# Performance work log

Measured on AMD Instinct MI355X. Metric: run time of the kernel, lower is better.

Reference implementation:

```python
import jax, jax.numpy as jnp
import numpy as np

B, S, IN, D, H, K, NLVL = 8, 1536, 32, 128, 4, 7, 2
DFF = 4 * D
DK = D // H
EPS = 1e-6


def setup_inputs() -> dict:
    key = jax.random.key(0)
    ks = jax.random.split(key, 24)
    rn = lambda k, sh, s=0.05: jax.random.normal(k, sh, jnp.float32) * s
    z = lambda sh: jnp.zeros(sh, jnp.float32)
    o = lambda sh: jnp.ones(sh, jnp.float32)
    return {
        'x': jax.random.normal(ks[0], (B, S, IN), jnp.float32),
        'enc_W': rn(ks[1], (IN, D)), 'enc_b': z((D,)),
        'ln_rnn_a': o((NLVL, D)), 'ln_rnn_b': z((NLVL, D)),
        'gru_Wih': rn(ks[2], (NLVL, 3 * D, D)), 'gru_Whh': rn(ks[3], (NLVL, 3 * D, D)),
        'gru_bih': z((NLVL, 3 * D)), 'gru_bhh': z((NLVL, 3 * D)),
        'ln_attn_a': o((NLVL, D)), 'ln_attn_b': z((NLVL, D)),
        'Wq': rn(ks[4], (NLVL, D, D)), 'bq': z((NLVL, D)),
        'Wk': rn(ks[5], (NLVL, D, D)), 'bk': z((NLVL, D)),
        'Wv': rn(ks[6], (NLVL, D, D)), 'bv': z((NLVL, D)),
        'Wo': rn(ks[7], (NLVL, D, D)), 'bo': z((NLVL, D)),
        'ln_ff_a': o((NLVL, D)), 'ln_ff_b': z((NLVL, D)),
        'ff_W1': rn(ks[8], (NLVL, D, DFF)), 'ff_b1': z((NLVL, DFF)),
        'ff_W2': rn(ks[9], (NLVL, DFF, D)), 'ff_b2': z((NLVL, D)),
        'out_W': rn(ks[10], (D, 1)), 'out_b': z((1,)),
    }


def layernorm(x, a, b):
    # faithful to torch code: unbiased std (ddof=1), divide by (std + eps)
    m = x.mean(-1, keepdims=True)
    s = jnp.std(x, axis=-1, ddof=1, keepdims=True)
    return a * (x - m) / (s + EPS) + b


def local_rnn(x, Wih, Whh, bih, bhh):
    # x: [B,S,D]. Window each position into its ksize-length causal window,
    # run a GRU over the window (scan over K steps, batched over B*S), keep last h.
    xp = jnp.pad(x, ((0, 0), (K - 1, 0), (0, 0)))            # zero left-pad
    win = jnp.stack([xp[:, i:i + S] for i in range(K)], 0)   # [K,B,S,D]

    def step(h, xt):
        gi = xt @ Wih.T + bih                                 # [B,S,3D]
        gh = h @ Whh.T + bhh
        ir, iz, inn = jnp.split(gi, 3, -1)
        hr, hz, hn = jnp.split(gh, 3, -1)
        r = jax.nn.sigmoid(ir + hr)
        zz = jax.nn.sigmoid(iz + hz)
        nn_ = jnp.tanh(inn + r * hn)
        return (1.0 - zz) * nn_ + zz * h, None

    h, _ = jax.lax.scan(step, jnp.zeros_like(x), win)
    return h


def mhpool(x, Wq, bq, Wk, bk, Wv, bv, Wo, bo):
    def heads(w, bb):
        return jnp.swapaxes((x @ w + bb).reshape(B, S, H, DK), 1, 2)  # [B,H,S,DK]
    q, k, v = heads(Wq, bq), heads(Wk, bk), heads(Wv, bv)
    scores = jnp.einsum('bhqd,bhkd->bhqk', q, k) / np.float32(np.sqrt(DK))
    mask = jnp.tril(jnp.ones((S, S), bool))
    scores = jnp.where(mask, scores, jnp.float32(-1e9))
    p = jax.nn.softmax(scores, axis=-1)
    o = jnp.einsum('bhqk,bhkd->bhqd', p, v)
    o = jnp.swapaxes(o, 1, 2).reshape(B, S, D)
    return o @ Wo + bo


def reference(x, enc_W, enc_b, ln_rnn_a, ln_rnn_b, gru_Wih, gru_Whh, gru_bih,
              gru_bhh, ln_attn_a, ln_attn_b, Wq, bq, Wk, bk, Wv, bv, Wo, bo,
              ln_ff_a, ln_ff_b, ff_W1, ff_b1, ff_W2, ff_b2, out_W, out_b):
    h = x @ enc_W + enc_b
    for i in range(NLVL):
        # LocalRNNLayer (pre-norm residual); LocalRNN.output Linear is unused in orig forward
        h = h + local_rnn(layernorm(h, ln_rnn_a[i], ln_rnn_b[i]),
                          gru_Wih[i], gru_Whh[i], gru_bih[i], gru_bhh[i])
        # MHPooling sublayer
        h = h + mhpool(layernorm(h, ln_attn_a[i], ln_attn_b[i]),
                       Wq[i], bq[i], Wk[i], bk[i], Wv[i], bv[i], Wo[i], bo[i])
        # PositionwiseFeedForward sublayer
        hn = layernorm(h, ln_ff_a[i], ln_ff_b[i])
        h = h + (jax.nn.relu(hn @ ff_W1[i] + ff_b1[i]) @ ff_W2[i] + ff_b2[i])
    return jax.nn.sigmoid(h @ out_W + out_b)
```

## Files before the change

kernel.cpp:

```cpp
#include <hip/hip_runtime.h>
#include <math.h>

#define DEV_INLINE __device__ __forceinline__

constexpr int B = 8, S = 1536, IN = 32, D = 128, NH = 4, KWIN = 7, NLVL = 2;
constexpr int DFF = 512, DKH = 32;
constexpr int M = B * S;
constexpr int MD = M * D;
constexpr float EPS = 1e-6f;

typedef unsigned short u16;
typedef __bf16 bf16x8 __attribute__((ext_vector_type(8)));
typedef float f32x4 __attribute__((ext_vector_type(4)));
typedef unsigned short u16x4 __attribute__((ext_vector_type(4)));

#define MFMA16(a, b, c) __builtin_amdgcn_mfma_f32_16x16x32_bf16(a, b, c, 0, 0, 0)

DEV_INLINE float sigmoidf_(float x) { return 1.f / (1.f + __expf(-x)); }

DEV_INLINE u16 f2bf(float f) {
    unsigned u = __builtin_bit_cast(unsigned, f);
    unsigned rnd = 0x7FFFu + ((u >> 16) & 1u);
    return (u16)((u + rnd) >> 16);
}
DEV_INLINE float b2f(u16 v) { return __builtin_bit_cast(float, (unsigned)v << 16); }

template <int KDIM>
DEV_INLINE void mfma_tile32(const u16* a0p, const u16* a1p, const u16* b0p, const u16* b1p,
                            f32x4& acc00, f32x4& acc01, f32x4& acc10, f32x4& acc11) {
    #pragma unroll
    for (int k0 = 0; k0 < KDIM; k0 += 32) {
        bf16x8 a0 = *(const bf16x8*)(a0p + k0);
        bf16x8 a1 = *(const bf16x8*)(a1p + k0);
        bf16x8 b0 = *(const bf16x8*)(b0p + k0);
        bf16x8 b1 = *(const bf16x8*)(b1p + k0);
        acc00 = MFMA16(a0, b0, acc00);
        acc01 = MFMA16(a0, b1, acc01);
        acc10 = MFMA16(a1, b0, acc10);
        acc11 = MFMA16(a1, b1, acc11);
    }
}

__global__ void k_prep(const float* __restrict__ Wih, const float* __restrict__ Whh,
                       const float* __restrict__ Wq, const float* __restrict__ Wk,
                       const float* __restrict__ Wv, const float* __restrict__ Wo,
                       const float* __restrict__ W1, const float* __restrict__ W2,
                       u16* __restrict__ Wih16, u16* __restrict__ Whh16,
                       u16* __restrict__ Wqkv, u16* __restrict__ WoT,
                       u16* __restrict__ W1T, u16* __restrict__ W2T) {
    constexpr int SZ_GRU = NLVL * 384 * 128;
    constexpr int SZ_DD  = NLVL * 128 * 128;
    constexpr int SZ_FF  = NLVL * 128 * 512;
    int i = blockIdx.x * 256 + threadIdx.x;
    if (i < SZ_GRU) { Wih16[i] = f2bf(Wih[i]); return; }
    i -= SZ_GRU;
    if (i < SZ_GRU) { Whh16[i] = f2bf(Whh[i]); return; }
    i -= SZ_GRU;
    if (i < 3 * SZ_DD) {
        int seg = i / SZ_DD, j = i - seg * SZ_DD;
        int lvl = j >> 14, rem = j & 16383, k = rem >> 7, n = rem & 127;
        const float* src = seg == 0 ? Wq : (seg == 1 ? Wk : Wv);
        Wqkv[(size_t)lvl * 384 * 128 + (size_t)(seg * 128 + n) * 128 + k] = f2bf(src[j]);
        return;
    }
    i -= 3 * SZ_DD;
    if (i < SZ_DD) {
        int lvl = i >> 14, rem = i & 16383, k = rem >> 7, n = rem & 127;
        WoT[(size_t)lvl * 16384 + n * 128 + k] = f2bf(Wo[i]); return;
    }
    i -= SZ_DD;
    if (i < SZ_FF) {
        int lvl = i >> 16, rem = i & 65535, k = rem >> 9, n = rem & 511;
        W1T[(size_t)lvl * 65536 + n * 128 + k] = f2bf(W1[i]); return;
    }
    i -= SZ_FF;
    if (i < SZ_FF) {
        int lvl = i >> 16, rem = i & 65535, k = rem >> 7, n = rem & 127;
        W2T[(size_t)lvl * 65536 + n * 512 + k] = f2bf(W2[i]); return;
    }
}

__global__ __launch_bounds__(256) void k_encoder(
    const float* __restrict__ x, const float* __restrict__ W, const float* __restrict__ b,
    const float* __restrict__ ga, const float* __restrict__ gb,
    float* __restrict__ h, u16* __restrict__ xnout) {
    __shared__ float xs[32][33];
    __shared__ float Ws[32][128];
    const int tid = threadIdx.x;
    const int row0 = blockIdx.x * 32;
    for (int i = tid; i < 32 * 32; i += 256) xs[i >> 5][i & 31] = x[(size_t)row0 * IN + i];
    for (int i = tid; i < 32 * 128; i += 256) Ws[i >> 7][i & 127] = W[i];
    __syncthreads();
    const int r = tid >> 3, cg = (tid & 7) * 16;
    float acc[16];
    #pragma unroll
    for (int j = 0; j < 16; ++j) acc[j] = b[cg + j];
    for (int k = 0; k < IN; ++k) {
        const float xv = xs[r][k];
        #pragma unroll
        for (int j = 0; j < 16; ++j) acc[j] = fmaf(xv, Ws[k][cg + j], acc[j]);
    }
    float s = 0.f;
    #pragma unroll
    for (int j = 0; j < 16; ++j) s += acc[j];
    s += __shfl_xor(s, 1); s += __shfl_xor(s, 2); s += __shfl_xor(s, 4);
    const float mean = s * (1.f / D);
    float q = 0.f;
    #pragma unroll
    for (int j = 0; j < 16; ++j) { float d = acc[j] - mean; q += d * d; }
    q += __shfl_xor(q, 1); q += __shfl_xor(q, 2); q += __shfl_xor(q, 4);
    const float inv = 1.f / (sqrtf(q * (1.f / (D - 1))) + EPS);
    float* hp = h + (size_t)(row0 + r) * D + cg;
    u16* xp = xnout + (size_t)(row0 + r) * D + cg;
    #pragma unroll
    for (int jj = 0; jj < 4; ++jj) {
        float4 hv = make_float4(acc[4 * jj], acc[4 * jj + 1], acc[4 * jj + 2], acc[4 * jj + 3]);
        *(float4*)(hp + 4 * jj) = hv;
        u16x4 o;
        #pragma unroll
        for (int c = 0; c < 4; ++c)
            o[c] = f2bf(ga[cg + 4 * jj + c] * (acc[4 * jj + c] - mean) * inv + gb[cg + 4 * jj + c]);
        *(u16x4*)(xp + 4 * jj) = o;
    }
}

__global__ __launch_bounds__(256) void k_gemm_qkv(
    const u16* __restrict__ A, const u16* __restrict__ Bqkv,
    const float* __restrict__ bq, const float* __restrict__ bk, const float* __restrict__ bv,
    u16* __restrict__ q16, u16* __restrict__ k16, u16* __restrict__ vt16) {
    constexpr float QS = 0.17677669529663687f * 1.4426950408889634f;
    const int wave = threadIdx.x >> 6, lane = threadIdx.x & 63;
    const int col16 = lane & 15, quad = lane >> 4;
    const int row0 = (blockIdx.x * 4 + wave) * 32;
    const int seg = blockIdx.y >> 2;
    const int c0 = (blockIdx.y & 3) * 32;
    const u16* a0p = A + (size_t)(row0 + col16) * 128 + quad * 8;
    const u16* b0p = Bqkv + (size_t)(seg * 128 + c0 + col16) * 128 + quad * 8;
    f32x4 acc00 = {0.f, 0.f, 0.f, 0.f}, acc01 = acc00, acc10 = acc00, acc11 = acc00;
    mfma_tile32<128>(a0p, a0p + 16 * 128, b0p, b0p + 16 * 128, acc00, acc01, acc10, acc11);
    const float* bias = seg == 0 ? bq : (seg == 1 ? bk : bv);
    const float bv0 = bias[c0 + col16];
    const float bv1 = bias[c0 + 16 + col16];
    if (seg < 2) {
        const float sc = seg == 0 ? QS : 1.f;
        u16* o16 = seg == 0 ? q16 : k16;
        #pragma unroll
        for (int r = 0; r < 4; ++r) {
            const size_t r0 = (size_t)(row0 + quad * 4 + r) * 128;
            const size_t r1 = r0 + 16 * 128;
            o16[r0 + c0 + col16]      = f2bf((acc00[r] + bv0) * sc);
            o16[r0 + c0 + 16 + col16] = f2bf((acc01[r] + bv1) * sc);
            o16[r1 + c0 + col16]      = f2bf((acc10[r] + bv0) * sc);
            o16[r1 + c0 + 16 + col16] = f2bf((acc11[r] + bv1) * sc);
        }
    } else {
        const int bb = row0 / S;
        const int ssv = row0 - bb * S;
        const int ca = c0 + col16, cb = c0 + 16 + col16;
        u16* pa = vt16 + ((size_t)((bb * NH + (ca >> 5)) * 32 + (ca & 31))) * S + ssv;
        u16* pb = vt16 + ((size_t)((bb * NH + (cb >> 5)) * 32 + (cb & 31))) * S + ssv;
        #pragma unroll
        for (int r = 0; r < 4; ++r) {
            const int lr = quad * 4 + r;
            pa[lr]      = f2bf(acc00[r] + bv0);
            pb[lr]      = f2bf(acc01[r] + bv1);
            pa[lr + 16] = f2bf(acc10[r] + bv0);
            pb[lr + 16] = f2bf(acc11[r] + bv1);
        }
    }
}

__global__ __launch_bounds__(512, 2) void k_gru_fused(
    const u16* __restrict__ xn,
    const u16* __restrict__ Wih16,
    const u16* __restrict__ Whh16,
    const float* __restrict__ bih, const float* __restrict__ bhh,
    float* __restrict__ hout,
    const float* __restrict__ ga, const float* __restrict__ gb,
    u16* __restrict__ xnaout) {
    constexpr int RB = 48;
    __shared__ __align__(16) u16 xnS[64 * 136];
    __shared__ __align__(16) u16 Gs[64 * 392];
    __shared__ __align__(16) u16 hs16[RB * 136];
    const int tid = threadIdx.x;
    const int wave = tid >> 6, lane = tid & 63;
    const int col16 = lane & 15, quad = lane >> 4;
    const int row0 = blockIdx.x * RB;
    const int ss0 = row0 % S;
    const int cc = wave * 16 + col16;

    for (int i = tid; i < 64 * 16; i += 512) {
        const int r = i >> 4, c8 = (i & 15) * 8;
        bf16x8 val = {};
        if (ss0 - 16 + r >= 0)
            val = *(const bf16x8*)(xn + (size_t)(row0 - 16 + r) * 128 + c8);
        *(bf16x8*)&xnS[r * 136 + c8] = val;
    }
    bf16x8 Breg[3][4];
    #pragma unroll
    for (int g = 0; g < 3; ++g)
        #pragma unroll
        for (int kc = 0; kc < 4; ++kc)
            Breg[g][kc] = *(const bf16x8*)(Whh16 + (size_t)(g * 128 + cc) * 128 + kc * 32 + quad * 8);
    float bi[3], bh[3];
    #pragma unroll
    for (int g = 0; g < 3; ++g) { bi[g] = bih[g * 128 + cc]; bh[g] = bhh[g * 128 + cc]; }
    __syncthreads();

    #pragma unroll
    for (int tt = wave; tt < 24; tt += 8) {
        const int rt = tt / 12, ct = tt - rt * 12;
        const u16* bp = Wih16 + (size_t)(ct * 32 + col16) * 128 + quad * 8;
        f32x4 a00 = {0.f, 0.f, 0.f, 0.f}, a01 = a00, a10 = a00, a11 = a00;
        #pragma unroll
        for (int k0 = 0; k0 < 128; k0 += 32) {
            bf16x8 af0 = *(const bf16x8*)&xnS[(rt * 32 + col16) * 136 + k0 + quad * 8];
            bf16x8 af1 = *(const bf16x8*)&xnS[(rt * 32 + 16 + col16) * 136 + k0 + quad * 8];
            bf16x8 b0 = *(const bf16x8*)(bp + k0);
            bf16x8 b1 = *(const bf16x8*)(bp + 16 * 128 + k0);
            a00 = MFMA16(af0, b0, a00);
            a01 = MFMA16(af0, b1, a01);
            a10 = MFMA16(af1, b0, a10);
            a11 = MFMA16(af1, b1, a11);
        }
        #pragma unroll
        for (int r = 0; r < 4; ++r) {
            const int gr0 = rt * 32 + quad * 4 + r, gr1 = gr0 + 16;
            Gs[gr0 * 392 + ct * 32 + col16]      = f2bf(a00[r]);
            Gs[gr0 * 392 + ct * 32 + 16 + col16] = f2bf(a01[r]);
            Gs[gr1 * 392 + ct * 32 + col16]      = f2bf(a10[r]);
            Gs[gr1 * 392 + ct * 32 + 16 + col16] = f2bf(a11[r]);
        }
    }
    float hp[12] = {};
    __syncthreads();

    for (int t = 0; t < KWIN; ++t) {
        const int shift = KWIN - 1 - t;
        f32x4 acc[3][3];
        #pragma unroll
        for (int rh = 0; rh < 3; ++rh)
            #pragma unroll
            for (int g = 0; g < 3; ++g) acc[rh][g] = {0.f, 0.f, 0.f, 0.f};
        if (t > 0) {
            bf16x8 af[3][4];
            #pragma unroll
            for (int rh = 0; rh < 3; ++rh)
                #pragma unroll
                for (int kc = 0; kc < 4; ++kc)
                    af[rh][kc] = *(const bf16x8*)&hs16[(rh * 16 + col16) * 136 + kc * 32 + quad * 8];
            __syncthreads();
            #pragma unroll
            for (int kc = 0; kc < 4; ++kc)
                #pragma unroll
                for (int g = 0; g < 3; ++g)
                    #pragma unroll
                    for (int rh = 0; rh < 3; ++rh)
                        acc[rh][g] = MFMA16(af[rh][kc], Breg[g][kc], acc[rh][g]);
        }
        const bool last = (t == KWIN - 1);
        #pragma unroll
        for (int rh = 0; rh < 3; ++rh) {
            #pragma unroll
            for (int r = 0; r < 4; ++r) {
                const int idx = rh * 4 + r;
                const int lrow = rh * 16 + quad * 4 + r;
                const int gr = lrow - shift + 16;
                const float xr  = b2f(Gs[gr * 392 + cc]);
                const float xz  = b2f(Gs[gr * 392 + 128 + cc]);
                const float xn_ = b2f(Gs[gr * 392 + 256 + cc]);
                const float rr = sigmoidf_(xr + bi[0] + acc[rh][0][r] + bh[0]);
                const float zz = sigmoidf_(xz + bi[1] + acc[rh][1][r] + bh[1]);
                const float e2 = __expf(2.f * (xn_ + bi[2] + rr * (acc[rh][2][r] + bh[2])));
                const float nn = 1.f - 2.f / (e2 + 1.f);
                const float hnew = (1.f - zz) * nn + zz * hp[idx];
                hp[idx] = hnew;
                if (!last) hs16[lrow * 136 + cc] = f2bf(hnew);
            }
        }
        __syncthreads();
    }
    float* hf = (float*)Gs;
    #pragma unroll
    for (int rh = 0; rh < 3; ++rh)
        #pragma unroll
        for (int r = 0; r < 4; ++r) {
            const int lrow = rh * 16 + quad * 4 + r;
            const float hv = hp[rh * 4 + r] + hout[(size_t)(row0 + lrow) * D + cc];
            hout[(size_t)(row0 + lrow) * D + cc] = hv;
            hf[lrow * 132 + cc] = hv;
        }
    __syncthreads();
    const int r = tid >> 3;
    if (r < RB) {
        const int cg = (tid & 7) * 16;
        float vals[16];
        #pragma unroll
        for (int jj = 0; jj < 4; ++jj) {
            float4 v = *(const float4*)&hf[r * 132 + cg + 4 * jj];
            vals[4 * jj] = v.x; vals[4 * jj + 1] = v.y; vals[4 * jj + 2] = v.z; vals[4 * jj + 3] = v.w;
        }
        float s = 0.f;
        #pragma unroll
        for (int j = 0; j < 16; ++j) s += vals[j];
        s += __shfl_xor(s, 1); s += __shfl_xor(s, 2); s += __shfl_xor(s, 4);
        const float mean = s * (1.f / D);
        float q = 0.f;
        #pragma unroll
        for (int j = 0; j < 16; ++j) { float d = vals[j] - mean; q += d * d; }
        q += __shfl_xor(q, 1); q += __shfl_xor(q, 2); q += __shfl_xor(q, 4);
        const float inv = 1.f / (sqrtf(q * (1.f / (D - 1))) + EPS);
        u16* xp = xnaout + (size_t)(row0 + r) * D + cg;
        #pragma unroll
        for (int jj = 0; jj < 4; ++jj) {
            u16x4 o;
            #pragma unroll
            for (int c = 0; c < 4; ++c)
                o[c] = f2bf(ga[cg + 4 * jj + c] * (vals[4 * jj + c] - mean) * inv + gb[cg + 4 * jj + c]);
            *(u16x4*)(xp + 4 * jj) = o;
        }
    }
}

__global__ __launch_bounds__(256) void k_attn_mfma(
    const u16* Qb, const u16* __restrict__ Kb,
    const u16* __restrict__ Vt, u16* O16) {
    const int wave = threadIdx.x >> 6, lane = threadIdx.x & 63;
    const int p = blockIdx.x;
    const int bh = blockIdx.y;
    const int b = bh >> 2, hh = bh & 3;
    const int col = lane & 15, quad = lane >> 4;

    __shared__ __align__(16) u16 Pb[4][32][40];
    __shared__ float Om[4][32][33];
    __shared__ float Lm[4][32];
    u16 (* __restrict__ P)[40] = Pb[wave];

    const u16* Kbase = Kb + (size_t)b * S * 128 + hh * 32;
    const u16* Vbase = Vt + (size_t)bh * 32 * S;

    #pragma unroll
    for (int half = 0; half < 2; ++half) {
        const int qt = half == 0 ? p : 47 - p;
        const int q0 = qt * 32;
        const int nkt = qt + 1;
        const u16* qp = Qb + (size_t)(b * S + q0 + col) * 128 + hh * 32 + quad * 8;
        const bf16x8 qf0 = *(const bf16x8*)qp;
        const bf16x8 qf1 = *(const bf16x8*)(qp + 16 * 128);
        f32x4 o00 = {0.f, 0.f, 0.f, 0.f}, o01 = o00, o10 = o00, o11 = o00;
        float lsum[8] = {};
        int kt = wave;
        bf16x8 kf0 = {}, kf1 = {}, vf0 = {}, vf1 = {};
        if (kt < nkt) {
            const u16* kp = Kbase + (size_t)(kt * 32 + col) * 128 + quad * 8;
            kf0 = *(const bf16x8*)kp;
            kf1 = *(const bf16x8*)(kp + 16 * 128);
            const u16* vp = Vbase + (size_t)col * S + kt * 32 + quad * 8;
            vf0 = *(const bf16x8*)vp;
            vf1 = *(const bf16x8*)(vp + 16 * S);
        }
        while (kt < nkt) {
            const int ktn = kt + 4;
            bf16x8 nk0 = kf0, nk1 = kf1, nv0 = vf0, nv1 = vf1;
            if (ktn < nkt) {
                const u16* kp = Kbase + (size_t)(ktn * 32 + col) * 128 + quad * 8;
                nk0 = *(const bf16x8*)kp;
                nk1 = *(const bf16x8*)(kp + 16 * 128);
                const u16* vp = Vbase + (size_t)col * S + ktn * 32 + quad * 8;
                nv0 = *(const bf16x8*)vp;
                nv1 = *(const bf16x8*)(vp + 16 * S);
            }
            f32x4 z = {0.f, 0.f, 0.f, 0.f};
            f32x4 s00 = MFMA16(qf0, kf0, z);
            f32x4 s01 = MFMA16(qf0, kf1, z);
            f32x4 s10 = MFMA16(qf1, kf0, z);
            f32x4 s11 = MFMA16(qf1, kf1, z);
            const bool diag = (kt == qt);
            const int k0g = kt * 32;
            #pragma unroll
            for (int r = 0; r < 4; ++r) {
                const int lr = quad * 4 + r;
                float p00 = __builtin_amdgcn_exp2f(s00[r]);
                float p01 = __builtin_amdgcn_exp2f(s01[r]);
                float p10 = __builtin_amdgcn_exp2f(s10[r]);
                float p11 = __builtin_amdgcn_exp2f(s11[r]);
                if (diag) {
                    const int qg0 = q0 + lr, qg1 = q0 + 16 + lr;
                    if (k0g + col > qg0)      p00 = 0.f;
                    if (k0g + 16 + col > qg0) p01 = 0.f;
                    if (k0g + col > qg1)      p10 = 0.f;
                    if (k0g + 16 + col > qg1) p11 = 0.f;
                }
                lsum[r]     += p00 + p01;
                lsum[4 + r] += p10 + p11;
                P[lr][col]           = f2bf(p00);
                P[lr][16 + col]      = f2bf(p01);
                P[16 + lr][col]      = f2bf(p10);
                P[16 + lr][16 + col] = f2bf(p11);
            }
            const bf16x8 pa0 = *(const bf16x8*)&P[col][quad * 8];
            const bf16x8 pa1 = *(const bf16x8*)&P[16 + col][quad * 8];
            o00 = MFMA16(pa0, vf0, o00);
            o01 = MFMA16(pa0, vf1, o01);
            o10 = MFMA16(pa1, vf0, o10);
            o11 = MFMA16(pa1, vf1, o11);
            kf0 = nk0; kf1 = nk1; vf0 = nv0; vf1 = nv1;
            kt = ktn;
        }
        #pragma unroll
        for (int i = 0; i < 8; ++i) {
            float v = lsum[i];
            v += __shfl_xor(v, 1); v += __shfl_xor(v, 2);
            v += __shfl_xor(v, 4); v += __shfl_xor(v, 8);
            lsum[i] = v;
        }
        #pragma unroll
        for (int r = 0; r < 4; ++r) {
            const int lr = quad * 4 + r;
            Om[wave][lr][col]           = o00[r];
            Om[wave][lr][16 + col]      = o01[r];
            Om[wave][16 + lr][col]      = o10[r];
            Om[wave][16 + lr][16 + col] = o11[r];
        }
        if (col == 0) {
            #pragma unroll
            for (int i = 0; i < 8; ++i)
                Lm[wave][(i >> 2) * 16 + quad * 4 + (i & 3)] = lsum[i];
        }
        __syncthreads();
        {
            const int tr = threadIdx.x >> 3, tc = (threadIdx.x & 7) * 4;
            const float inv = 1.f / (Lm[0][tr] + Lm[1][tr] + Lm[2][tr] + Lm[3][tr]);
            u16x4 outv;
            #pragma unroll
            for (int c = 0; c < 4; ++c) {
                const float o = Om[0][tr][tc + c] + Om[1][tr][tc + c] +
                                Om[2][tr][tc + c] + Om[3][tr][tc + c];
                outv[c] = f2bf(o * inv);
            }
            *(u16x4*)(O16 + (size_t)(b * S + q0 + tr) * 128 + hh * 32 + tc) = outv;
        }
        __syncthreads();
    }
}

template <bool LAST>
__global__ __launch_bounds__(256) void k_mho_ffn(
    const u16* __restrict__ ao, const u16* __restrict__ WoT, const float* __restrict__ bo,
    float* __restrict__ hio,
    const float* __restrict__ ga1, const float* __restrict__ gb1,
    const u16* __restrict__ W1T, const float* __restrict__ b1,
    const u16* __restrict__ W2T, const float* __restrict__ b2,
    const float* __restrict__ ga2, const float* __restrict__ gb2, u16* __restrict__ xnout,
    const float* __restrict__ outW, const float* __restrict__ outb, float* __restrict__ outp) {
    __shared__ float hL[32 * 132];
    __shared__ __align__(16) u16 xnL[32 * 136];
    __shared__ __align__(16) u16 Ls[32 * 520];
    const int tid = threadIdx.x;
    const int wave = tid >> 6, lane = tid & 63;
    const int col16 = lane & 15, quad = lane >> 4;
    const int row0 = blockIdx.x * 32;
    const int c0 = wave * 32;

    {
        const u16* a0p = ao + (size_t)(row0 + col16) * 128 + quad * 8;
        const u16* b0p = WoT + (size_t)(c0 + col16) * 128 + quad * 8;
        f32x4 acc00 = {0.f, 0.f, 0.f, 0.f}, acc01 = acc00, acc10 = acc00, acc11 = acc00;
        mfma_tile32<128>(a0p, a0p + 16 * 128, b0p, b0p + 16 * 128, acc00, acc01, acc10, acc11);
        const float bv0 = bo[c0 + col16];
        const float bv1 = bo[c0 + 16 + col16];
        #pragma unroll
        for (int r = 0; r < 4; ++r) {
            const int l0 = quad * 4 + r, l1 = 16 + quad * 4 + r;
            const size_t g0 = (size_t)(row0 + l0) * D, g1 = (size_t)(row0 + l1) * D;
            hL[l0 * 132 + c0 + col16]      = acc00[r] + bv0 + hio[g0 + c0 + col16];
            hL[l0 * 132 + c0 + 16 + col16] = acc01[r] + bv1 + hio[g0 + c0 + 16 + col16];
            hL[l1 * 132 + c0 + col16]      = acc10[r] + bv0 + hio[g1 + c0 + col16];
            hL[l1 * 132 + c0 + 16 + col16] = acc11[r] + bv1 + hio[g1 + c0 + 16 + col16];
        }
    }
    __syncthreads();
    {
        const int r = tid >> 3, cg = (tid & 7) * 16;
        float vals[16];
        #pragma unroll
        for (int jj = 0; jj < 4; ++jj) {
            float4 v = *(const float4*)&hL[r * 132 + cg + 4 * jj];
            vals[4 * jj] = v.x; vals[4 * jj + 1] = v.y; vals[4 * jj + 2] = v.z; vals[4 * jj + 3] = v.w;
        }
        float s = 0.f;
        #pragma unroll
        for (int j = 0; j < 16; ++j) s += vals[j];
        s += __shfl_xor(s, 1); s += __shfl_xor(s, 2); s += __shfl_xor(s, 4);
        const float mean = s * (1.f / D);
        float q = 0.f;
        #pragma unroll
        for (int j = 0; j < 16; ++j) { float d = vals[j] - mean; q += d * d; }
        q += __shfl_xor(q, 1); q += __shfl_xor(q, 2); q += __shfl_xor(q, 4);
        const float inv = 1.f / (sqrtf(q * (1.f / (D - 1))) + EPS);
        #pragma unroll
        for (int jj = 0; jj < 4; ++jj) {
            u16x4 o;
            #pragma unroll
            for (int c = 0; c < 4; ++c)
                o[c] = f2bf(ga1[cg + 4 * jj + c] * (vals[4 * jj + c] - mean) * inv + gb1[cg + 4 * jj + c]);
            *(u16x4*)&xnL[r * 136 + cg + 4 * jj] = o;
        }
    }
    __syncthreads();
    #pragma unroll
    for (int ct = 0; ct < 4; ++ct) {
        const int c0f = wave * 128 + ct * 32;
        const u16* b0p = W1T + (size_t)(c0f + col16) * 128 + quad * 8;
        f32x4 acc00 = {0.f, 0.f, 0.f, 0.f}, acc01 = acc00, acc10 = acc00, acc11 = acc00;
        #pragma unroll
        for (int k0 = 0; k0 < 128; k0 += 32) {
            bf16x8 a0 = *(const bf16x8*)&xnL[col16 * 136 + k0 + quad * 8];
            bf16x8 a1 = *(const bf16x8*)&xnL[(16 + col16) * 136 + k0 + quad * 8];
            bf16x8 b0 = *(const bf16x8*)(b0p + k0);
            bf16x8 b1 = *(const bf16x8*)(b0p + 16 * 128 + k0);
            acc00 = MFMA16(a0, b0, acc00);
            acc01 = MFMA16(a0, b1, acc01);
            acc10 = MFMA16(a1, b0, acc10);
            acc11 = MFMA16(a1, b1, acc11);
        }
        const float bv0 = b1[c0f + col16];
        const float bv1 = b1[c0f + 16 + col16];
        #pragma unroll
        for (int r = 0; r < 4; ++r) {
            const int l0 = quad * 4 + r, l1 = 16 + quad * 4 + r;
            Ls[l0 * 520 + c0f + col16]      = f2bf(fmaxf(acc00[r] + bv0, 0.f));
            Ls[l0 * 520 + c0f + 16 + col16] = f2bf(fmaxf(acc01[r] + bv1, 0.f));
            Ls[l1 * 520 + c0f + col16]      = f2bf(fmaxf(acc10[r] + bv0, 0.f));
            Ls[l1 * 520 + c0f + 16 + col16] = f2bf(fmaxf(acc11[r] + bv1, 0.f));
        }
    }
    __syncthreads();
    {
        f32x4 acc00 = {0.f, 0.f, 0.f, 0.f}, acc01 = acc00, acc10 = acc00, acc11 = acc00;
        #pragma unroll
        for (int k0 = 0; k0 < 512; k0 += 32) {
            bf16x8 a0 = *(const bf16x8*)&Ls[col16 * 520 + k0 + quad * 8];
            bf16x8 a1 = *(const bf16x8*)&Ls[(16 + col16) * 520 + k0 + quad * 8];
            const u16* bp = W2T + (size_t)(c0 + col16) * 512 + k0 + quad * 8;
            bf16x8 b0 = *(const bf16x8*)bp;
            bf16x8 b1v = *(const bf16x8*)(bp + 16 * 512);
            acc00 = MFMA16(a0, b0, acc00);
            acc01 = MFMA16(a0, b1v, acc01);
            acc10 = MFMA16(a1, b0, acc10);
            acc11 = MFMA16(a1, b1v, acc11);
        }
        const float bv0 = b2[c0 + col16];
        const float bv1 = b2[c0 + 16 + col16];
        #pragma unroll
        for (int r = 0; r < 4; ++r) {
            const int l0 = quad * 4 + r, l1 = 16 + quad * 4 + r;
            const size_t g0 = (size_t)(row0 + l0) * D, g1 = (size_t)(row0 + l1) * D;
            const float v00 = acc00[r] + bv0 + hL[l0 * 132 + c0 + col16];
            const float v01 = acc01[r] + bv1 + hL[l0 * 132 + c0 + 16 + col16];
            const float v10 = acc10[r] + bv0 + hL[l1 * 132 + c0 + col16];
            const float v11 = acc11[r] + bv1 + hL[l1 * 132 + c0 + 16 + col16];
            hio[g0 + c0 + col16]      = v00;
            hio[g0 + c0 + 16 + col16] = v01;
            hio[g1 + c0 + col16]      = v10;
            hio[g1 + c0 + 16 + col16] = v11;
            hL[l0 * 132 + c0 + col16]      = v00;
            hL[l0 * 132 + c0 + 16 + col16] = v01;
            hL[l1 * 132 + c0 + col16]      = v10;
            hL[l1 * 132 + c0 + 16 + col16] = v11;
        }
    }
    __syncthreads();
    {
        const int r = tid >> 3, cg = (tid & 7) * 16;
        float vals[16];
        #pragma unroll
        for (int jj = 0; jj < 4; ++jj) {
            float4 v = *(const float4*)&hL[r * 132 + cg + 4 * jj];
            vals[4 * jj] = v.x; vals[4 * jj + 1] = v.y; vals[4 * jj + 2] = v.z; vals[4 * jj + 3] = v.w;
        }
        if constexpr (LAST) {
            float dot = 0.f;
            #pragma unroll
            for (int j = 0; j < 16; ++j) dot += vals[j] * outW[cg + j];
            dot += __shfl_xor(dot, 1); dot += __shfl_xor(dot, 2); dot += __shfl_xor(dot, 4);
            if ((tid & 7) == 0) outp[row0 + r] = sigmoidf_(dot + outb[0]);
        } else {
            float s = 0.f;
            #pragma unroll
            for (int j = 0; j < 16; ++j) s += vals[j];
            s += __shfl_xor(s, 1); s += __shfl_xor(s, 2); s += __shfl_xor(s, 4);
            const float mean = s * (1.f / D);
            float q = 0.f;
            #pragma unroll
            for (int j = 0; j < 16; ++j) { float d = vals[j] - mean; q += d * d; }
            q += __shfl_xor(q, 1); q += __shfl_xor(q, 2); q += __shfl_xor(q, 4);
            const float inv = 1.f / (sqrtf(q * (1.f / (D - 1))) + EPS);
            u16* xp = xnout + (size_t)(row0 + r) * D + cg;
            #pragma unroll
            for (int jj = 0; jj < 4; ++jj) {
                u16x4 o;
                #pragma unroll
                for (int c = 0; c < 4; ++c)
                    o[c] = f2bf(ga2[cg + 4 * jj + c] * (vals[4 * jj + c] - mean) * inv + gb2[cg + 4 * jj + c]);
                *(u16x4*)(xp + 4 * jj) = o;
            }
        }
    }
}

extern "C" void kernel_launch(void* const* d_in, const int* in_sizes, int n_in,
                              void* d_out, int out_size, void* d_ws, size_t ws_size,
                              hipStream_t stream) {
    const float* x       = (const float*)d_in[0];
    const float* enc_W   = (const float*)d_in[1];
    const float* enc_b   = (const float*)d_in[2];
    const float* ln_rnn_a = (const float*)d_in[3];
    const float* ln_rnn_b = (const float*)d_in[4];
    const float* gru_Wih = (const float*)d_in[5];
    const float* gru_Whh = (const float*)d_in[6];
    const float* gru_bih = (const float*)d_in[7];
    const float* gru_bhh = (const float*)d_in[8];
    const float* ln_attn_a = (const float*)d_in[9];
    const float* ln_attn_b = (const float*)d_in[10];
    const float* Wq = (const float*)d_in[11];
    const float* bq = (const float*)d_in[12];
    const float* Wk = (const float*)d_in[13];
    const float* bk = (const float*)d_in[14];
    const float* Wv = (const float*)d_in[15];
    const float* bv = (const float*)d_in[16];
    const float* Wo = (const float*)d_in[17];
    const float* bo = (const float*)d_in[18];
    const float* ln_ff_a = (const float*)d_in[19];
    const float* ln_ff_b = (const float*)d_in[20];
    const float* ff_W1 = (const float*)d_in[21];
    const float* ff_b1 = (const float*)d_in[22];
    const float* ff_W2 = (const float*)d_in[23];
    const float* ff_b2 = (const float*)d_in[24];
    const float* out_W = (const float*)d_in[25];
    const float* out_b = (const float*)d_in[26];

    float* h   = (float*)d_ws;
    u16* pool  = (u16*)(h + MD);
    u16* xn16  = pool + (size_t)4 * MD;
    u16* Wih16 = xn16 + MD;
    u16* Whh16 = Wih16 + NLVL * 384 * D;
    u16* Wqkv  = Whh16 + NLVL * 384 * D;
    u16* WoT   = Wqkv + NLVL * 384 * D;
    u16* W1T   = WoT + NLVL * D * D;
    u16* W2T   = W1T + NLVL * D * DFF;

    u16* q16   = pool;
    u16* k16   = pool + MD;
    u16* vt16  = pool + (size_t)2 * MD;
    u16* xna16 = pool + (size_t)3 * MD;
    u16* ao16  = q16;

    k_prep<<<2304, 256, 0, stream>>>(gru_Wih, gru_Whh, Wq, Wk, Wv, Wo, ff_W1, ff_W2,
                                     Wih16, Whh16, Wqkv, WoT, W1T, W2T);
    k_encoder<<<M / 32, 256, 0, stream>>>(x, enc_W, enc_b, ln_rnn_a, ln_rnn_b, h, xn16);

    for (int lvl = 0; lvl < NLVL; ++lvl) {
        k_gru_fused<<<256, 512, 0, stream>>>(
            xn16, Wih16 + lvl * 384 * D, Whh16 + lvl * 384 * D,
            gru_bih + lvl * 384, gru_bhh + lvl * 384,
            h, ln_attn_a + lvl * D, ln_attn_b + lvl * D, xna16);

        k_gemm_qkv<<<dim3(96, 12), 256, 0, stream>>>(
            xna16, Wqkv + lvl * 384 * D, bq + lvl * D, bk + lvl * D, bv + lvl * D,
            q16, k16, vt16);
        k_attn_mfma<<<dim3(24, 32), 256, 0, stream>>>(q16, k16, vt16, ao16);

        if (lvl + 1 < NLVL) {
            k_mho_ffn<false><<<M / 32, 256, 0, stream>>>(
                ao16, WoT + lvl * D * D, bo + lvl * D, h,
                ln_ff_a + lvl * D, ln_ff_b + lvl * D,
                W1T + lvl * D * DFF, ff_b1 + lvl * DFF,
                W2T + lvl * DFF * D, ff_b2 + lvl * D,
                ln_rnn_a + (lvl + 1) * D, ln_rnn_b + (lvl + 1) * D, xn16,
                nullptr, nullptr, nullptr);
        } else {
            k_mho_ffn<true><<<M / 32, 256, 0, stream>>>(
                ao16, WoT + lvl * D * D, bo + lvl * D, h,
                ln_ff_a + lvl * D, ln_ff_b + lvl * D,
                W1T + lvl * D * DFF, ff_b1 + lvl * DFF,
                W2T + lvl * DFF * D, ff_b2 + lvl * D,
                nullptr, nullptr, nullptr,
                out_W, out_b, (float*)d_out);
        }
    }
}
```

Before: 322.7 us.

## Fuse QKV projection into GRU kernel and merge weight prep with encoder

The separate QKV GEMM kernel is removed. The GRU kernel now writes its layer-normed output into shared memory and computes the Q, K and V projections there with MFMA, writing q16, k16 and transposed V directly. This avoids a global round trip of the normalized activations and one launch per level. Weight conversion and the encoder are also merged into one launch using block-index dispatch, which removes another launch. The cost is that the QKV work now runs inside the GRU kernel, which is limited to 256 blocks and has heavy LDS use, so that GEMM gets less parallelism and the kernel may see more register pressure.

```diff
diff --git a/kernel.cpp b/kernel.cpp
--- a/kernel.cpp
+++ b/kernel.cpp
@@ -41,60 +41,61 @@
     }
 }
 
-__global__ void k_prep(const float* __restrict__ Wih, const float* __restrict__ Whh,
-                       const float* __restrict__ Wq, const float* __restrict__ Wk,
-                       const float* __restrict__ Wv, const float* __restrict__ Wo,
-                       const float* __restrict__ W1, const float* __restrict__ W2,
-                       u16* __restrict__ Wih16, u16* __restrict__ Whh16,
-                       u16* __restrict__ Wqkv, u16* __restrict__ WoT,
-                       u16* __restrict__ W1T, u16* __restrict__ W2T) {
-    constexpr int SZ_GRU = NLVL * 384 * 128;
-    constexpr int SZ_DD  = NLVL * 128 * 128;
-    constexpr int SZ_FF  = NLVL * 128 * 512;
-    int i = blockIdx.x * 256 + threadIdx.x;
-    if (i < SZ_GRU) { Wih16[i] = f2bf(Wih[i]); return; }
-    i -= SZ_GRU;
-    if (i < SZ_GRU) { Whh16[i] = f2bf(Whh[i]); return; }
-    i -= SZ_GRU;
-    if (i < 3 * SZ_DD) {
-        int seg = i / SZ_DD, j = i - seg * SZ_DD;
-        int lvl = j >> 14, rem = j & 16383, k = rem >> 7, n = rem & 127;
-        const float* src = seg == 0 ? Wq : (seg == 1 ? Wk : Wv);
-        Wqkv[(size_t)lvl * 384 * 128 + (size_t)(seg * 128 + n) * 128 + k] = f2bf(src[j]);
-        return;
-    }
-    i -= 3 * SZ_DD;
-    if (i < SZ_DD) {
-        int lvl = i >> 14, rem = i & 16383, k = rem >> 7, n = rem & 127;
-        WoT[(size_t)lvl * 16384 + n * 128 + k] = f2bf(Wo[i]); return;
-    }
-    i -= SZ_DD;
-    if (i < SZ_FF) {
-        int lvl = i >> 16, rem = i & 65535, k = rem >> 9, n = rem & 511;
-        W1T[(size_t)lvl * 65536 + n * 128 + k] = f2bf(W1[i]); return;
-    }
-    i -= SZ_FF;
-    if (i < SZ_FF) {
-        int lvl = i >> 16, rem = i & 65535, k = rem >> 7, n = rem & 127;
-        W2T[(size_t)lvl * 65536 + n * 512 + k] = f2bf(W2[i]); return;
-    }
-}
-
-__global__ __launch_bounds__(256) void k_encoder(
-    const float* __restrict__ x, const float* __restrict__ W, const float* __restrict__ b,
+__global__ __launch_bounds__(256) void k_prep_enc(
+    const float* __restrict__ Wih, const float* __restrict__ Whh,
+    const float* __restrict__ Wq, const float* __restrict__ Wk,
+    const float* __restrict__ Wv, const float* __restrict__ Wo,
+    const float* __restrict__ W1, const float* __restrict__ W2,
+    u16* __restrict__ Wih16, u16* __restrict__ Whh16,
+    u16* __restrict__ Wqkv, u16* __restrict__ WoT,
+    u16* __restrict__ W1T, u16* __restrict__ W2T,
+    const float* __restrict__ x, const float* __restrict__ encW, const float* __restrict__ encb,
     const float* __restrict__ ga, const float* __restrict__ gb,
     float* __restrict__ h, u16* __restrict__ xnout) {
     __shared__ float xs[32][33];
     __shared__ float Ws[32][128];
     const int tid = threadIdx.x;
-    const int row0 = blockIdx.x * 32;
+    if (blockIdx.x < 2304) {
+        constexpr int SZ_GRU = NLVL * 384 * 128;
+        constexpr int SZ_DD  = NLVL * 128 * 128;
+        constexpr int SZ_FF  = NLVL * 128 * 512;
+        int i = blockIdx.x * 256 + tid;
+        if (i < SZ_GRU) { Wih16[i] = f2bf(Wih[i]); return; }
+        i -= SZ_GRU;
+        if (i < SZ_GRU) { Whh16[i] = f2bf(Whh[i]); return; }
+        i -= SZ_GRU;
+        if (i < 3 * SZ_DD) {
+            int seg = i / SZ_DD, j = i - seg * SZ_DD;
+            int lvl = j >> 14, rem = j & 16383, k = rem >> 7, n = rem & 127;
+            const float* src = seg == 0 ? Wq : (seg == 1 ? Wk : Wv);
+            Wqkv[(size_t)lvl * 384 * 128 + (size_t)(seg * 128 + n) * 128 + k] = f2bf(src[j]);
+            return;
+        }
+        i -= 3 * SZ_DD;
+        if (i < SZ_DD) {
+            int lvl = i >> 14, rem = i & 16383, k = rem >> 7, n = rem & 127;
+            WoT[(size_t)lvl * 16384 + n * 128 + k] = f2bf(Wo[i]); return;
+        }
+        i -= SZ_DD;
+        if (i < SZ_FF) {
+            int lvl = i >> 16, rem = i & 65535, k = rem >> 9, n = rem & 511;
+            W1T[(size_t)lvl * 65536 + n * 128 + k] = f2bf(W1[i]); return;
+        }
+        i -= SZ_FF;
+        if (i < SZ_FF) {
+            int lvl = i >> 16, rem = i & 65535, k = rem >> 7, n = rem & 127;
+            W2T[(size_t)lvl * 65536 + n * 512 + k] = f2bf(W2[i]); return;
+        }
+        return;
+    }
+    const int row0 = (blockIdx.x - 2304) * 32;
     for (int i = tid; i < 32 * 32; i += 256) xs[i >> 5][i & 31] = x[(size_t)row0 * IN + i];
-    for (int i = tid; i < 32 * 128; i += 256) Ws[i >> 7][i & 127] = W[i];
+    for (int i = tid; i < 32 * 128; i += 256) Ws[i >> 7][i & 127] = encW[i];
     __syncthreads();
     const int r = tid >> 3, cg = (tid & 7) * 16;
     float acc[16];
     #pragma unroll
-    for (int j = 0; j < 16; ++j) acc[j] = b[cg + j];
+    for (int j = 0; j < 16; ++j) acc[j] = encb[cg + j];
     for (int k = 0; k < IN; ++k) {
         const float xv = xs[r][k];
         #pragma unroll
@@ -124,61 +125,18 @@
     }
 }
 
-__global__ __launch_bounds__(256) void k_gemm_qkv(
-    const u16* __restrict__ A, const u16* __restrict__ Bqkv,
-    const float* __restrict__ bq, const float* __restrict__ bk, const float* __restrict__ bv,
-    u16* __restrict__ q16, u16* __restrict__ k16, u16* __restrict__ vt16) {
-    constexpr float QS = 0.17677669529663687f * 1.4426950408889634f;
-    const int wave = threadIdx.x >> 6, lane = threadIdx.x & 63;
-    const int col16 = lane & 15, quad = lane >> 4;
-    const int row0 = (blockIdx.x * 4 + wave) * 32;
-    const int seg = blockIdx.y >> 2;
-    const int c0 = (blockIdx.y & 3) * 32;
-    const u16* a0p = A + (size_t)(row0 + col16) * 128 + quad * 8;
-    const u16* b0p = Bqkv + (size_t)(seg * 128 + c0 + col16) * 128 + quad * 8;
-    f32x4 acc00 = {0.f, 0.f, 0.f, 0.f}, acc01 = acc00, acc10 = acc00, acc11 = acc00;
-    mfma_tile32<128>(a0p, a0p + 16 * 128, b0p, b0p + 16 * 128, acc00, acc01, acc10, acc11);
-    const float* bias = seg == 0 ? bq : (seg == 1 ? bk : bv);
-    const float bv0 = bias[c0 + col16];
-    const float bv1 = bias[c0 + 16 + col16];
-    if (seg < 2) {
-        const float sc = seg == 0 ? QS : 1.f;
-        u16* o16 = seg == 0 ? q16 : k16;
-        #pragma unroll
-        for (int r = 0; r < 4; ++r) {
-            const size_t r0 = (size_t)(row0 + quad * 4 + r) * 128;
-            const size_t r1 = r0 + 16 * 128;
-            o16[r0 + c0 + col16]      = f2bf((acc00[r] + bv0) * sc);
-            o16[r0 + c0 + 16 + col16] = f2bf((acc01[r] + bv1) * sc);
-            o16[r1 + c0 + col16]      = f2bf((acc10[r] + bv0) * sc);
-            o16[r1 + c0 + 16 + col16] = f2bf((acc11[r] + bv1) * sc);
-        }
-    } else {
-        const int bb = row0 / S;
-        const int ssv = row0 - bb * S;
-        const int ca = c0 + col16, cb = c0 + 16 + col16;
-        u16* pa = vt16 + ((size_t)((bb * NH + (ca >> 5)) * 32 + (ca & 31))) * S + ssv;
-        u16* pb = vt16 + ((size_t)((bb * NH + (cb >> 5)) * 32 + (cb & 31))) * S + ssv;
-        #pragma unroll
-        for (int r = 0; r < 4; ++r) {
-            const int lr = quad * 4 + r;
-            pa[lr]      = f2bf(acc00[r] + bv0);
-            pb[lr]      = f2bf(acc01[r] + bv1);
-            pa[lr + 16] = f2bf(acc10[r] + bv0);
-            pb[lr + 16] = f2bf(acc11[r] + bv1);
-        }
-    }
-}
-
-__global__ __launch_bounds__(512, 2) void k_gru_fused(
+__global__ __launch_bounds__(512, 2) void k_gru_qkv(
     const u16* __restrict__ xn,
     const u16* __restrict__ Wih16,
     const u16* __restrict__ Whh16,
     const float* __restrict__ bih, const float* __restrict__ bhh,
     float* __restrict__ hout,
     const float* __restrict__ ga, const float* __restrict__ gb,
-    u16* __restrict__ xnaout) {
+    const u16* __restrict__ Wqkv,
+    const float* __restrict__ bq, const float* __restrict__ bk, const float* __restrict__ bv,
+    u16* __restrict__ q16, u16* __restrict__ k16, u16* __restrict__ vt16) {
     constexpr int RB = 48;
+    constexpr float QS = 0.17677669529663687f * 1.4426950408889634f;
     __shared__ __align__(16) u16 xnS[64 * 136];
     __shared__ __align__(16) u16 Gs[64 * 392];
     __shared__ __align__(16) u16 hs16[RB * 136];
@@ -291,33 +249,73 @@
             hf[lrow * 132 + cc] = hv;
         }
     __syncthreads();
-    const int r = tid >> 3;
-    if (r < RB) {
-        const int cg = (tid & 7) * 16;
-        float vals[16];
-        #pragma unroll
-        for (int jj = 0; jj < 4; ++jj) {
-            float4 v = *(const float4*)&hf[r * 132 + cg + 4 * jj];
-            vals[4 * jj] = v.x; vals[4 * jj + 1] = v.y; vals[4 * jj + 2] = v.z; vals[4 * jj + 3] = v.w;
-        }
-        float s = 0.f;
-        #pragma unroll
-        for (int j = 0; j < 16; ++j) s += vals[j];
-        s += __shfl_xor(s, 1); s += __shfl_xor(s, 2); s += __shfl_xor(s, 4);
-        const float mean = s * (1.f / D);
-        float q = 0.f;
-        #pragma unroll
-        for (int j = 0; j < 16; ++j) { float d = vals[j] - mean; q += d * d; }
-        q += __shfl_xor(q, 1); q += __shfl_xor(q, 2); q += __shfl_xor(q, 4);
-        const float inv = 1.f / (sqrtf(q * (1.f / (D - 1))) + EPS);
-        u16* xp = xnaout + (size_t)(row0 + r) * D + cg;
-        #pragma unroll
-        for (int jj = 0; jj < 4; ++jj) {
-            u16x4 o;
-            #pragma unroll
-            for (int c = 0; c < 4; ++c)
-                o[c] = f2bf(ga[cg + 4 * jj + c] * (vals[4 * jj + c] - mean) * inv + gb[cg + 4 * jj + c]);
-            *(u16x4*)(xp + 4 * jj) = o;
+    {
+        const int r = tid >> 3;
+        if (r < RB) {
+            const int cg = (tid & 7) * 16;
+            float vals[16];
+            #pragma unroll
+            for (int jj = 0; jj < 4; ++jj) {
+                float4 v = *(const float4*)&hf[r * 132 + cg + 4 * jj];
+                vals[4 * jj] = v.x; vals[4 * jj + 1] = v.y; vals[4 * jj + 2] = v.z; vals[4 * jj + 3] = v.w;
+            }
+            float s = 0.f;
+            #pragma unroll
+            for (int j = 0; j < 16; ++j) s += vals[j];
+            s += __shfl_xor(s, 1); s += __shfl_xor(s, 2); s += __shfl_xor(s, 4);
+            const float mean = s * (1.f / D);
+            float q = 0.f;
+            #pragma unroll
+            for (int j = 0; j < 16; ++j) { float d = vals[j] - mean; q += d * d; }
+            q += __shfl_xor(q, 1); q += __shfl_xor(q, 2); q += __shfl_xor(q, 4);
+            const float inv = 1.f / (sqrtf(q * (1.f / (D - 1))) + EPS);
+            #pragma unroll
+            for (int jj = 0; jj < 4; ++jj) {
+                u16x4 o;
+                #pragma unroll
+                for (int c = 0; c < 4; ++c)
+                    o[c] = f2bf(ga[cg + 4 * jj + c] * (vals[4 * jj + c] - mean) * inv + gb[cg + 4 * jj + c]);
+                *(u16x4*)&hs16[r * 136 + cg + 4 * jj] = o;
+            }
+        }
+    }
+    __syncthreads();
+    for (int tt = wave; tt < 36; tt += 8) {
+        const int rt = tt / 12, ct = tt - rt * 12;
+        const int seg = ct >> 2;
+        const int c0 = (ct & 3) * 32;
+        const u16* bp = Wqkv + (size_t)(seg * 128 + c0 + col16) * 128 + quad * 8;
+        f32x4 a0 = {0.f, 0.f, 0.f, 0.f}, a1 = a0;
+        #pragma unroll
+        for (int k0 = 0; k0 < 128; k0 += 32) {
+            bf16x8 af = *(const bf16x8*)&hs16[(rt * 16 + col16) * 136 + k0 + quad * 8];
+            bf16x8 b0 = *(const bf16x8*)(bp + k0);
+            bf16x8 b1 = *(const bf16x8*)(bp + 16 * 128 + k0);
+            a0 = MFMA16(af, b0, a0);
+            a1 = MFMA16(af, b1, a1);
+        }
+        if (seg < 2) {
+            const float* bias = seg == 0 ? bq : bk;
+            const float sc = seg == 0 ? QS : 1.f;
+            const float bv0 = bias[c0 + col16], bv1 = bias[c0 + 16 + col16];
+            u16* o16 = seg == 0 ? q16 : k16;
+            #pragma unroll
+            for (int r = 0; r < 4; ++r) {
+                const size_t gr = (size_t)(row0 + rt * 16 + quad * 4 + r) * 128;
+                o16[gr + c0 + col16]      = f2bf((a0[r] + bv0) * sc);
+                o16[gr + c0 + 16 + col16] = f2bf((a1[r] + bv1) * sc);
+            }
+        } else {
+            const float bv0 = bv[c0 + col16], bv1 = bv[c0 + 16 + col16];
+            const int bb = row0 / S, ssv = row0 - bb * S + rt * 16;
+            const int ca = c0 + col16, cb = c0 + 16 + col16;
+            u16* pa = vt16 + ((size_t)((bb * NH + (ca >> 5)) * 32 + (ca & 31))) * S + ssv;
+            u16* pb = vt16 + ((size_t)((bb * NH + (cb >> 5)) * 32 + (cb & 31))) * S + ssv;
+            #pragma unroll
+            for (int r = 0; r < 4; ++r) {
+                pa[quad * 4 + r] = f2bf(a0[r] + bv0);
+                pb[quad * 4 + r] = f2bf(a1[r] + bv1);
+            }
         }
     }
 }
@@ -642,7 +640,7 @@
 
     float* h   = (float*)d_ws;
     u16* pool  = (u16*)(h + MD);
-    u16* xn16  = pool + (size_t)4 * MD;
+    u16* xn16  = pool + (size_t)3 * MD;
     u16* Wih16 = xn16 + MD;
     u16* Whh16 = Wih16 + NLVL * 384 * D;
     u16* Wqkv  = Whh16 + NLVL * 384 * D;
@@ -653,22 +651,21 @@
     u16* q16   = pool;
     u16* k16   = pool + MD;
     u16* vt16  = pool + (size_t)2 * MD;
-    u16* xna16 = pool + (size_t)3 * MD;
     u16* ao16  = q16;
 
-    k_prep<<<2304, 256, 0, stream>>>(gru_Wih, gru_Whh, Wq, Wk, Wv, Wo, ff_W1, ff_W2,
-                                     Wih16, Whh16, Wqkv, WoT, W1T, W2T);
-    k_encoder<<<M / 32, 256, 0, stream>>>(x, enc_W, enc_b, ln_rnn_a, ln_rnn_b, h, xn16);
+    k_prep_enc<<<2688, 256, 0, stream>>>(
+        gru_Wih, gru_Whh, Wq, Wk, Wv, Wo, ff_W1, ff_W2,
+        Wih16, Whh16, Wqkv, WoT, W1T, W2T,
+        x, enc_W, enc_b, ln_rnn_a, ln_rnn_b, h, xn16);
 
     for (int lvl = 0; lvl < NLVL; ++lvl) {
-        k_gru_fused<<<256, 512, 0, stream>>>(
+        k_gru_qkv<<<256, 512, 0, stream>>>(
             xn16, Wih16 + lvl * 384 * D, Whh16 + lvl * 384 * D,
             gru_bih + lvl * 384, gru_bhh + lvl * 384,
-            h, ln_attn_a + lvl * D, ln_attn_b + lvl * D, xna16);
-
-        k_gemm_qkv<<<dim3(96, 12), 256, 0, stream>>>(
-            xna16, Wqkv + lvl * 384 * D, bq + lvl * D, bk + lvl * D, bv + lvl * D,
+            h, ln_attn_a + lvl * D, ln_attn_b + lvl * D,
+            Wqkv + lvl * 384 * D, bq + lvl * D, bk + lvl * D, bv + lvl * D,
             q16, k16, vt16);
+
         k_attn_mfma<<<dim3(24, 32), 256, 0, stream>>>(q16, k16, vt16, ao16);
 
         if (lvl + 1 < NLVL) {
```

Measured after the change: 320.0 us. Within noise of the previous version (-0.9%).
